# Kernel optimization log

Hardware: AMD Instinct MI355X
Metric: run time of the kernel (lower is better)

## Reference

```python
import jax, jax.numpy as jnp
import numpy as np

K = 27  # 3^3 kernel offsets for kernel_size=3, D=3
N_DOWN, N_UP = 40000, 160000
C_DOWN, C_SKIP, C_OUT = 128, 64, 96


def setup_inputs() -> dict:
    key = jax.random.key(0)
    ks = jax.random.split(key, 8)
    skip_feat = jax.random.normal(ks[0], (N_UP, C_SKIP), dtype=jnp.float32)
    down_feat = jax.random.normal(ks[1], (N_DOWN, C_DOWN), dtype=jnp.float32)
    W_deconv = jax.random.normal(ks[2], (K, C_DOWN, C_DOWN), dtype=jnp.float32) * (1.0 / np.sqrt(C_DOWN * K))
    W_conv = jax.random.normal(ks[3], (K, C_SKIP + C_DOWN, C_OUT), dtype=jnp.float32) * (1.0 / np.sqrt((C_SKIP + C_DOWN) * K))
    deconv_in_idx = jax.random.randint(ks[4], (K, N_DOWN), 0, N_DOWN, dtype=jnp.int32)
    deconv_out_idx = jax.random.randint(ks[5], (K, N_DOWN), 0, N_UP, dtype=jnp.int32)
    conv_in_idx = jax.random.randint(ks[6], (K, N_UP), 0, N_UP, dtype=jnp.int32)
    conv_out_idx = jax.random.randint(ks[7], (K, N_UP), 0, N_UP, dtype=jnp.int32)
    return {
        "skip_feat": skip_feat,
        "down_feat": down_feat,
        "W_deconv": W_deconv,
        "W_conv": W_conv,
        "deconv_in_idx": deconv_in_idx,
        "deconv_out_idx": deconv_out_idx,
        "conv_in_idx": conv_in_idx,
        "conv_out_idx": conv_out_idx,
    }


def _sparse_conv(feat, W, in_idx, out_idx, n_out):
    """ME-style sparse conv: per-offset gather -> matmul -> scatter-add."""
    out = jnp.zeros((n_out, W.shape[2]), dtype=feat.dtype)
    for k in range(W.shape[0]):  # fixed small loop over 27 kernel offsets
        msg = feat[in_idx[k]] @ W[k]          # [E_k, C_out]
        out = out.at[out_idx[k]].add(msg)
    return out


def reference(skip_feat, down_feat, W_deconv, W_conv,
              deconv_in_idx, deconv_out_idx, conv_in_idx, conv_out_idx):
    n_up = skip_feat.shape[0]
    # transposed sparse conv (stride 2) + ReLU
    up_feat = jax.nn.relu(_sparse_conv(down_feat, W_deconv, deconv_in_idx, deconv_out_idx, n_up))
    # ME.cat(up_feat, skip_feat): channel concat on shared coordinates
    cat_feat = jnp.concatenate([up_feat, skip_feat], axis=1)  # [N_up, C_down+C_skip]
    # sparse conv (stride 1) + ReLU
    net = jax.nn.relu(_sparse_conv(cat_feat, W_conv, conv_in_idx, conv_out_idx, n_up))
    return net
```

## Files before the change

### kernel.cpp

```cpp
#include <hip/hip_runtime.h>
#include <cstdint>

#define K_OFF 27
#define NDOWN 40000
#define NUP   160000
#define CDOWN 128
#define CSKIP 64
#define CCAT  192
#define COUT  96
#define TM    64
#define MT_D  5
#define MT_C  10

typedef __bf16 bf16x8 __attribute__((ext_vector_type(8)));
typedef float f32x4 __attribute__((ext_vector_type(4)));

__device__ __forceinline__ unsigned short f2b(float f) {
    unsigned int u = __float_as_uint(f);
    u += 0x7FFFu + ((u >> 16) & 1u);
    return (unsigned short)(u >> 16);
}
__device__ __forceinline__ unsigned int pk2(float a, float b) {
    return (unsigned)f2b(a) | ((unsigned)f2b(b) << 16);
}

__device__ __forceinline__ void gll16(const void* gsrc, void* ldst) {
    auto g = reinterpret_cast<const __attribute__((address_space(1))) unsigned int*>(
        reinterpret_cast<uintptr_t>(gsrc));
    auto l = reinterpret_cast<__attribute__((address_space(3))) unsigned int*>(
        reinterpret_cast<uintptr_t>(ldst));
    __builtin_amdgcn_global_load_lds(g, l, 16, 0, 0);
}


__global__ void pack_down_kernel(const float* __restrict__ down,
                                 unsigned short* __restrict__ dbf) {
    int i = blockIdx.x * 256 + threadIdx.x;
    if (i >= NDOWN * CDOWN / 8) return;
    const float4* s = (const float4*)down + (long)i * 2;
    float4 v0 = s[0], v1 = s[1];
    uint4 o;
    o.x = pk2(v0.x, v0.y); o.y = pk2(v0.z, v0.w);
    o.z = pk2(v1.x, v1.y); o.w = pk2(v1.z, v1.w);
    ((uint4*)dbf)[i] = o;
}

__global__ void pack_w_kernel(const float* __restrict__ Wd, const float* __restrict__ Wc,
                              unsigned short* __restrict__ WdT, unsigned short* __restrict__ WcT) {
    int i = blockIdx.x * 256 + threadIdx.x;
    if (i < K_OFF * CDOWN * CDOWN) {
        int k = i / (CDOWN * CDOWN), rem = i % (CDOWN * CDOWN);
        int n = rem >> 7, c = rem & 127;
        WdT[i] = f2b(Wd[((long)k * CDOWN + c) * CDOWN + n]);
    }
    if (i < K_OFF * COUT * CCAT) {
        int k = i / (COUT * CCAT), rem = i % (COUT * CCAT);
        int n = rem / CCAT, c = rem % CCAT;
        WcT[i] = f2b(Wc[((long)k * CCAT + c) * COUT + n]);
    }
}

__global__ void pack_cat_kernel(const float* __restrict__ up, const float* __restrict__ skip,
                                unsigned short* __restrict__ cat) {
    const int t = threadIdx.x;
    const int j = blockIdx.x * 8 + t / 24;
    const int s = t % 24;
    const int e0 = s * 8;
    float4 v0, v1;
    if (e0 < CDOWN) {
        const float4* src = (const float4*)(up + (long)j * CDOWN + e0);
        v0 = src[0]; v1 = src[1];
        v0.x = fmaxf(v0.x, 0.f); v0.y = fmaxf(v0.y, 0.f);
        v0.z = fmaxf(v0.z, 0.f); v0.w = fmaxf(v0.w, 0.f);
        v1.x = fmaxf(v1.x, 0.f); v1.y = fmaxf(v1.y, 0.f);
        v1.z = fmaxf(v1.z, 0.f); v1.w = fmaxf(v1.w, 0.f);
    } else {
        const float4* src = (const float4*)(skip + (long)j * CSKIP + (e0 - CDOWN));
        v0 = src[0]; v1 = src[1];
    }
    uint4 o;
    o.x = pk2(v0.x, v0.y); o.y = pk2(v0.z, v0.w);
    o.z = pk2(v1.x, v1.y); o.w = pk2(v1.z, v1.w);
    ((uint4*)(cat + (long)j * CCAT))[s] = o;
}

__global__ __launch_bounds__(256, 2)
void deconv_fast(const unsigned short* __restrict__ dbf,
                 const unsigned short* __restrict__ WdT,
                 const int* __restrict__ in_idx,
                 const int* __restrict__ out_idx,
                 float* __restrict__ up) {
    __shared__ __align__(1024) unsigned short sA[TM * CDOWN];

    const int segs = (NDOWN / TM) / MT_D;
    const int bk = blockIdx.x / segs;
    const int tile0 = (blockIdx.x % segs) * MT_D;
    const int t = threadIdx.x;
    const int wave = t >> 6, lane = t & 63;
    const int col = lane & 15, quad = lane >> 4;
    const int wm = wave & 1, wn = wave >> 1;

    int srow[4], soff[4];
#pragma unroll
    for (int i = 0; i < 4; i++) {
        int c = wave * 256 + i * 64 + lane;
        int r = c >> 4, cc = c & 15;
        srow[i] = r;
        soff[i] = (cc ^ (r & 7)) * 16;
    }

    bf16x8 b[4][4];
    {
        const unsigned short* wb = WdT + (long)bk * CDOWN * CDOWN;
#pragma unroll
        for (int kk = 0; kk < 4; kk++)
#pragma unroll
            for (int nt = 0; nt < 4; nt++)
                b[kk][nt] = *(const bf16x8*)&wb[(wn * 64 + nt * 16 + col) * CDOWN + kk * 32 + quad * 8];
    }

    const long kBase = (long)bk * NDOWN;
    const char* sAc = (const char*)sA;

    for (int tt = 0; tt < MT_D; ++tt) {
        const int rowbase = (tile0 + tt) * TM;
#pragma unroll
        for (int i = 0; i < 4; i++) {
            const int j = in_idx[kBase + rowbase + srow[i]];
            gll16((const char*)dbf + (long)j * (CDOWN * 2) + soff[i],
                  (char*)sA + (wave * 4 + i) * 1024);
        }
        __syncthreads();

        f32x4 acc[2][4];
#pragma unroll
        for (int mi = 0; mi < 2; mi++)
#pragma unroll
            for (int nt = 0; nt < 4; nt++) acc[mi][nt] = (f32x4){0.f, 0.f, 0.f, 0.f};

#pragma unroll
        for (int kk = 0; kk < 4; kk++) {
            const int ch = kk * 4 + quad;
#pragma unroll
            for (int mi = 0; mi < 2; mi++) {
                const int row = wm * 32 + mi * 16 + col;
                bf16x8 a = *(const bf16x8*)(sAc + row * 256 + ((ch ^ (row & 7)) * 16));
#pragma unroll
                for (int nt = 0; nt < 4; nt++)
                    acc[mi][nt] = __builtin_amdgcn_mfma_f32_16x16x32_bf16(a, b[kk][nt], acc[mi][nt], 0, 0, 0);
            }
        }
        __syncthreads();

#pragma unroll
        for (int mi = 0; mi < 2; mi++)
#pragma unroll
            for (int r = 0; r < 4; r++) {
                const int lrow = wm * 32 + mi * 16 + quad * 4 + r;
                const long ob = (long)out_idx[kBase + rowbase + lrow] * CDOWN;
#pragma unroll
                for (int nt = 0; nt < 4; nt++)
                    atomicAdd(&up[ob + wn * 64 + nt * 16 + col], acc[mi][nt][r]);
            }
    }
}

__global__ __launch_bounds__(256, 2)
void conv_fast(const unsigned short* __restrict__ cat,
               const unsigned short* __restrict__ WcT,
               const int* __restrict__ in_idx,
               const int* __restrict__ out_idx,
               float* __restrict__ out) {
    __shared__ __align__(1024) unsigned short sA[TM * CCAT];

    const int segs = (NUP / TM) / MT_C;
    const int bk = blockIdx.x / segs;
    const int tile0 = (blockIdx.x % segs) * MT_C;
    const int t = threadIdx.x;
    const int wave = t >> 6, lane = t & 63;
    const int col = lane & 15, quad = lane >> 4;
    const int wm = wave & 1, wn = wave >> 1;

    int srow[6], soff[6];
#pragma unroll
    for (int i = 0; i < 6; i++) {
        int c = wave * 384 + i * 64 + lane;
        int r = c / 24, cc = c % 24;
        srow[i] = r;
        soff[i] = (cc ^ (r & 7)) * 16;
    }

    bf16x8 b[6][3];
    {
        const unsigned short* wb = WcT + (long)bk * COUT * CCAT;
#pragma unroll
        for (int kk = 0; kk < 6; kk++)
#pragma unroll
            for (int nt = 0; nt < 3; nt++)
                b[kk][nt] = *(const bf16x8*)&wb[(wn * 48 + nt * 16 + col) * CCAT + kk * 32 + quad * 8];
    }

    const long kBase = (long)bk * NUP;
    const char* sAc = (const char*)sA;

    for (int tt = 0; tt < MT_C; ++tt) {
        const int rowbase = (tile0 + tt) * TM;
#pragma unroll
        for (int i = 0; i < 6; i++) {
            const int j = in_idx[kBase + rowbase + srow[i]];
            gll16((const char*)cat + (long)j * (CCAT * 2) + soff[i],
                  (char*)sA + (wave * 6 + i) * 1024);
        }
        __syncthreads();

        f32x4 acc[2][3];
#pragma unroll
        for (int mi = 0; mi < 2; mi++)
#pragma unroll
            for (int nt = 0; nt < 3; nt++) acc[mi][nt] = (f32x4){0.f, 0.f, 0.f, 0.f};

#pragma unroll
        for (int kk = 0; kk < 6; kk++) {
            const int ch = kk * 4 + quad;
#pragma unroll
            for (int mi = 0; mi < 2; mi++) {
                const int row = wm * 32 + mi * 16 + col;
                bf16x8 a = *(const bf16x8*)(sAc + row * 384 + ((ch ^ (row & 7)) * 16));
#pragma unroll
                for (int nt = 0; nt < 3; nt++)
                    acc[mi][nt] = __builtin_amdgcn_mfma_f32_16x16x32_bf16(a, b[kk][nt], acc[mi][nt], 0, 0, 0);
            }
        }
        __syncthreads();

#pragma unroll
        for (int mi = 0; mi < 2; mi++)
#pragma unroll
            for (int r = 0; r < 4; r++) {
                const int lrow = wm * 32 + mi * 16 + quad * 4 + r;
                const long ob = (long)out_idx[kBase + rowbase + lrow] * COUT;
#pragma unroll
                for (int nt = 0; nt < 3; nt++)
                    atomicAdd(&out[ob + wn * 48 + nt * 16 + col], acc[mi][nt][r]);
            }
    }
}

#define SA1 136
#define SB1 136

__global__ __launch_bounds__(256, 2)
void deconv_kernel(const float* __restrict__ down,
                   const float* __restrict__ Wd,
                   const int* __restrict__ in_idx,
                   const int* __restrict__ out_idx,
                   float* __restrict__ up) {
    __shared__ __align__(16) unsigned short sA[TM * SA1];
    __shared__ __align__(16) unsigned short sB[CDOWN * SB1];
    __shared__ int sOut[TM];

    const int tiles = NDOWN / TM;
    const int bk = blockIdx.x / tiles;
    const int tile = blockIdx.x % tiles;
    const int t = threadIdx.x;
    const long kInBase = (long)bk * NDOWN + tile * TM;

    {
        const int r = t >> 2;
        const int c0 = (t & 3) * 32;
        const int j = in_idx[kInBase + r];
        const float* src = down + (long)j * CDOWN + c0;
        unsigned short* dst = sA + r * SA1 + c0;
        #pragma unroll
        for (int c = 0; c < 32; c += 4) {
            float4 v = *(const float4*)(src + c);
            *(unsigned int*)(dst + c)     = pk2(v.x, v.y);
            *(unsigned int*)(dst + c + 2) = pk2(v.z, v.w);
        }
    }
    {
        const float* wsrc = Wd + (long)bk * CDOWN * CDOWN;
        for (int idx = t; idx < CDOWN * CDOWN; idx += 256) {
            const int kk = idx >> 7;
            const int n  = idx & 127;
            sB[n * SB1 + kk] = f2b(wsrc[idx]);
        }
    }
    if (t < TM) sOut[t] = out_idx[kInBase + t];
    __syncthreads();

    const int wave = t >> 6;
    const int lane = t & 63;
    const int col  = lane & 15;
    const int quad = lane >> 4;
    const int mrow = wave * 16 + col;

    f32x4 acc[8];
    #pragma unroll
    for (int i = 0; i < 8; i++) acc[i] = (f32x4){0.f, 0.f, 0.f, 0.f};

    #pragma unroll
    for (int k0 = 0; k0 < CDOWN; k0 += 32) {
        const int koff = k0 + quad * 8;
        bf16x8 a = *(const bf16x8*)&sA[mrow * SA1 + koff];
        #pragma unroll
        for (int nt = 0; nt < 8; nt++) {
            bf16x8 bb = *(const bf16x8*)&sB[(nt * 16 + col) * SB1 + koff];
            acc[nt] = __builtin_amdgcn_mfma_f32_16x16x32_bf16(a, bb, acc[nt], 0, 0, 0);
        }
    }
    #pragma unroll
    for (int r = 0; r < 4; r++) {
        const int lrow = wave * 16 + quad * 4 + r;
        const long obase = (long)sOut[lrow] * CDOWN;
        #pragma unroll
        for (int nt = 0; nt < 8; nt++)
            atomicAdd(&up[obase + nt * 16 + col], acc[nt][r]);
    }
}

#define SA2 200
#define SB2 200

__global__ __launch_bounds__(256, 2)
void conv_kernel(const float* __restrict__ up,
                 const float* __restrict__ skip,
                 const float* __restrict__ Wc,
                 const int* __restrict__ in_idx,
                 const int* __restrict__ out_idx,
                 float* __restrict__ out) {
    __shared__ __align__(16) unsigned short sA[TM * SA2];
    __shared__ __align__(16) unsigned short sB[COUT * SB2];
    __shared__ int sOut[TM];

    const int tiles = NUP / TM;
    const int bk = blockIdx.x / tiles;
    const int tile = blockIdx.x % tiles;
    const int t = threadIdx.x;
    const long kInBase = (long)bk * NUP + tile * TM;

    {
        const int r = t >> 2;
        const int c0 = (t & 3) * 48;
        const int j = in_idx[kInBase + r];
        const float* uprow = up + (long)j * CDOWN;
        const float* skrow = skip + (long)j * CSKIP;
        unsigned short* dst = sA + r * SA2 + c0;
        #pragma unroll
        for (int c = 0; c < 48; c += 4) {
            const int gc = c0 + c;
            float4 v;
            if (gc < CDOWN) {
                v = *(const float4*)(uprow + gc);
                v.x = fmaxf(v.x, 0.f); v.y = fmaxf(v.y, 0.f);
                v.z = fmaxf(v.z, 0.f); v.w = fmaxf(v.w, 0.f);
            } else {
                v = *(const float4*)(skrow + (gc - CDOWN));
            }
            *(unsigned int*)(dst + c)     = pk2(v.x, v.y);
            *(unsigned int*)(dst + c + 2) = pk2(v.z, v.w);
        }
    }
    {
        const float* wsrc = Wc + (long)bk * CCAT * COUT;
        for (int idx = t; idx < CCAT * COUT; idx += 256) {
            const int kk = idx / COUT;
            const int n  = idx - kk * COUT;
            sB[n * SB2 + kk] = f2b(wsrc[idx]);
        }
    }
    if (t < TM) sOut[t] = out_idx[kInBase + t];
    __syncthreads();

    const int wave = t >> 6;
    const int lane = t & 63;
    const int col  = lane & 15;
    const int quad = lane >> 4;
    const int mrow = wave * 16 + col;

    f32x4 acc[6];
    #pragma unroll
    for (int i = 0; i < 6; i++) acc[i] = (f32x4){0.f, 0.f, 0.f, 0.f};

    #pragma unroll
    for (int k0 = 0; k0 < CCAT; k0 += 32) {
        const int koff = k0 + quad * 8;
        bf16x8 a = *(const bf16x8*)&sA[mrow * SA2 + koff];
        #pragma unroll
        for (int nt = 0; nt < 6; nt++) {
            bf16x8 bb = *(const bf16x8*)&sB[(nt * 16 + col) * SB2 + koff];
            acc[nt] = __builtin_amdgcn_mfma_f32_16x16x32_bf16(a, bb, acc[nt], 0, 0, 0);
        }
    }
    #pragma unroll
    for (int r = 0; r < 4; r++) {
        const int lrow = wave * 16 + quad * 4 + r;
        const long obase = (long)sOut[lrow] * COUT;
        #pragma unroll
        for (int nt = 0; nt < 6; nt++)
            atomicAdd(&out[obase + nt * 16 + col], acc[nt][r]);
    }
}

__global__ void relu_kernel(float* __restrict__ x, int n4) {
    int i = blockIdx.x * blockDim.x + threadIdx.x;
    if (i < n4) {
        float4 v = ((float4*)x)[i];
        v.x = fmaxf(v.x, 0.f); v.y = fmaxf(v.y, 0.f);
        v.z = fmaxf(v.z, 0.f); v.w = fmaxf(v.w, 0.f);
        ((float4*)x)[i] = v;
    }
}

extern "C" void kernel_launch(void* const* d_in, const int* in_sizes, int n_in,
                              void* d_out, int out_size, void* d_ws, size_t ws_size,
                              hipStream_t stream) {
    const float* skip   = (const float*)d_in[0];
    const float* down   = (const float*)d_in[1];
    const float* Wd     = (const float*)d_in[2];
    const float* Wc     = (const float*)d_in[3];
    const int* dc_in    = (const int*)d_in[4];
    const int* dc_out   = (const int*)d_in[5];
    const int* cv_in    = (const int*)d_in[6];
    const int* cv_out   = (const int*)d_in[7];
    float* out = (float*)d_out;
    float* up  = (float*)d_ws;

    const size_t OFF_CAT = (size_t)NUP * CDOWN * 4;
    const size_t OFF_DBF = OFF_CAT + (size_t)NUP * CCAT * 2;
    const size_t OFF_WDT = OFF_DBF + (size_t)NDOWN * CDOWN * 2;
    const size_t OFF_WCT = OFF_WDT + (size_t)K_OFF * CDOWN * CDOWN * 2;
    const size_t WS_NEED = OFF_WCT + (size_t)K_OFF * COUT * CCAT * 2;

    hipMemsetAsync(up, 0, (size_t)NUP * CDOWN * sizeof(float), stream);
    hipMemsetAsync(out, 0, (size_t)out_size * sizeof(float), stream);

    if (ws_size >= WS_NEED) {
        unsigned short* catb = (unsigned short*)((char*)d_ws + OFF_CAT);
        unsigned short* dbf  = (unsigned short*)((char*)d_ws + OFF_DBF);
        unsigned short* WdT  = (unsigned short*)((char*)d_ws + OFF_WDT);
        unsigned short* WcT  = (unsigned short*)((char*)d_ws + OFF_WCT);

        pack_down_kernel<<<(NDOWN * CDOWN / 8 + 255) / 256, 256, 0, stream>>>(down, dbf);
        pack_w_kernel<<<(K_OFF * COUT * CCAT + 255) / 256, 256, 0, stream>>>(Wd, Wc, WdT, WcT);
        deconv_fast<<<K_OFF * ((NDOWN / TM) / MT_D), 256, 0, stream>>>(dbf, WdT, dc_in, dc_out, up);
        pack_cat_kernel<<<NUP / 8, 192, 0, stream>>>(up, skip, catb);
        conv_fast<<<K_OFF * ((NUP / TM) / MT_C), 256, 0, stream>>>(catb, WcT, cv_in, cv_out, out);
    } else {
        deconv_kernel<<<K_OFF * (NDOWN / TM), 256, 0, stream>>>(down, Wd, dc_in, dc_out, up);
        conv_kernel<<<K_OFF * (NUP / TM), 256, 0, stream>>>(up, skip, Wc, cv_in, cv_out, out);
    }
    relu_kernel<<<(out_size / 4 + 255) / 256, 256, 0, stream>>>(out, out_size / 4);
}
```

Measured before the change: 1.921 ms.

## Invert conv scatter into CSR gather with pre-summed inputs and fused ReLU

Builds a per-offset CSR of conv edges grouped by output row, using a histogram, a multi-level scan and a scatter. The new conv kernel walks all 27 offsets for one tile of output rows. Because the matmul is linear, it sums in fp32 all input rows that land on the same output row for an offset, then runs one MFMA pass per offset. Output is written directly with ReLU applied, so the float atomics, the output memset and the separate ReLU kernel go away. The trade-offs are extra sort kernels, reuse of the dead up buffer and the output buffer as scratch, rounding of the summed inputs to bf16, and weight reloads into LDS for every offset.

```diff
diff --git a/kernel.cpp b/kernel.cpp
--- a/kernel.cpp
+++ b/kernel.cpp
@@ -10,7 +10,7 @@
 #define COUT  96
 #define TM    64
 #define MT_D  5
-#define MT_C  10
+#define B_BINS (K_OFF * NUP)
 
 typedef __bf16 bf16x8 __attribute__((ext_vector_type(8)));
 typedef float f32x4 __attribute__((ext_vector_type(4)));
@@ -22,6 +22,9 @@
 }
 __device__ __forceinline__ unsigned int pk2(float a, float b) {
     return (unsigned)f2b(a) | ((unsigned)f2b(b) << 16);
+}
+__device__ __forceinline__ float b2f(unsigned int lo16) {
+    return __uint_as_float(lo16 << 16);
 }
 
 __device__ __forceinline__ void gll16(const void* gsrc, void* ldst) {
@@ -31,7 +34,6 @@
         reinterpret_cast<uintptr_t>(ldst));
     __builtin_amdgcn_global_load_lds(g, l, 16, 0, 0);
 }
-
 
 __global__ void pack_down_kernel(const float* __restrict__ down,
                                  unsigned short* __restrict__ dbf) {
@@ -165,85 +167,174 @@
     }
 }
 
+__global__ void hist_kernel(const int* __restrict__ cv_out, unsigned int* __restrict__ hist) {
+    const int i = blockIdx.x * 256 + threadIdx.x;
+    const int k = blockIdx.y;
+    const int j = cv_out[(long)k * NUP + i];
+    atomicAdd(&hist[(long)k * NUP + j], 1u);
+}
+
+__global__ void scan_blocks(const unsigned int* __restrict__ in, unsigned int* __restrict__ out,
+                            unsigned int* __restrict__ aux, int n) {
+    __shared__ unsigned int ls[256];
+    const int t = threadIdx.x;
+    const long base = (long)blockIdx.x * 1024 + (long)t * 4;
+    unsigned int v0 = (base     < n) ? in[base]     : 0u;
+    unsigned int v1 = (base + 1 < n) ? in[base + 1] : 0u;
+    unsigned int v2 = (base + 2 < n) ? in[base + 2] : 0u;
+    unsigned int v3 = (base + 3 < n) ? in[base + 3] : 0u;
+    const unsigned int s = v0 + v1 + v2 + v3;
+    ls[t] = s;
+    __syncthreads();
+    for (int off = 1; off < 256; off <<= 1) {
+        unsigned int x = (t >= off) ? ls[t - off] : 0u;
+        __syncthreads();
+        ls[t] += x;
+        __syncthreads();
+    }
+    const unsigned int ex = ls[t] - s;
+    if (base     < n) out[base]     = ex;
+    if (base + 1 < n) out[base + 1] = ex + v0;
+    if (base + 2 < n) out[base + 2] = ex + v0 + v1;
+    if (base + 3 < n) out[base + 3] = ex + v0 + v1 + v2;
+    if (aux != nullptr && t == 255) aux[blockIdx.x] = ls[255];
+}
+
+__global__ void addback_kernel(unsigned int* __restrict__ out, const unsigned int* __restrict__ aux, int n) {
+    const long i = (long)blockIdx.x * 256 + threadIdx.x;
+    if (i < n) out[i] += aux[i >> 10];
+}
+
+__global__ void scatter_kernel(const int* __restrict__ cv_in,
+                               const int* __restrict__ cv_out,
+                               const unsigned int* __restrict__ start,
+                               unsigned int* __restrict__ hist,
+                               unsigned int* __restrict__ entries) {
+    const int i = blockIdx.x * 256 + threadIdx.x;
+    const int k = blockIdx.y;
+    const long p = (long)k * NUP + i;
+    const int j = cv_out[p];
+    const long bin = (long)k * NUP + j;
+    const unsigned int off = atomicSub(&hist[bin], 1u) - 1u;
+    entries[start[bin] + off] = (unsigned int)cv_in[p];
+}
+
 __global__ __launch_bounds__(256, 2)
-void conv_fast(const unsigned short* __restrict__ cat,
-               const unsigned short* __restrict__ WcT,
-               const int* __restrict__ in_idx,
-               const int* __restrict__ out_idx,
-               float* __restrict__ out) {
+void conv_inv(const unsigned short* __restrict__ cat,
+              const unsigned short* __restrict__ WcT,
+              const unsigned int* __restrict__ start,
+              const unsigned int* __restrict__ entries,
+              float* __restrict__ out) {
     __shared__ __align__(1024) unsigned short sA[TM * CCAT];
-
-    const int segs = (NUP / TM) / MT_C;
-    const int bk = blockIdx.x / segs;
-    const int tile0 = (blockIdx.x % segs) * MT_C;
+    __shared__ __align__(1024) unsigned short sB[COUT * CCAT];
+
+    const int j0 = blockIdx.x * TM;
     const int t = threadIdx.x;
     const int wave = t >> 6, lane = t & 63;
     const int col = lane & 15, quad = lane >> 4;
     const int wm = wave & 1, wn = wave >> 1;
-
-    int srow[6], soff[6];
-#pragma unroll
-    for (int i = 0; i < 6; i++) {
-        int c = wave * 384 + i * 64 + lane;
-        int r = c / 24, cc = c % 24;
-        srow[i] = r;
-        soff[i] = (cc ^ (r & 7)) * 16;
-    }
-
-    bf16x8 b[6][3];
-    {
-        const unsigned short* wb = WcT + (long)bk * COUT * CCAT;
-#pragma unroll
-        for (int kk = 0; kk < 6; kk++)
+    const int r  = t >> 2;
+    const int cq = (t & 3) * 6;
+
+    f32x4 acc[2][3];
+#pragma unroll
+    for (int mi = 0; mi < 2; mi++)
+#pragma unroll
+        for (int nt = 0; nt < 3; nt++) acc[mi][nt] = (f32x4){0.f, 0.f, 0.f, 0.f};
+
+    char* sAc = (char*)sA;
+    char* sBc = (char*)sB;
+
+    for (int k = 0; k < K_OFF; k++) {
+        const long kb = (long)k * NUP;
+        const unsigned int s0 = start[kb + j0 + r];
+        const long i1 = kb + j0 + r + 1;
+        const unsigned int s1 = (i1 == (long)B_BINS) ? (unsigned int)B_BINS : start[i1];
+        const int n = (int)(s1 - s0);
+
+        uint4 ch[6];
+        if (n == 1) {
+            const unsigned int ie = entries[s0];
+            const uint4* src = (const uint4*)(cat + (long)ie * CCAT) + cq;
+#pragma unroll
+            for (int q = 0; q < 6; q++) ch[q] = src[q];
+        } else if (n == 0) {
+#pragma unroll
+            for (int q = 0; q < 6; q++) ch[q] = make_uint4(0u, 0u, 0u, 0u);
+        } else {
+            float fa[6][8];
+#pragma unroll
+            for (int q = 0; q < 6; q++)
+#pragma unroll
+                for (int e8 = 0; e8 < 8; e8++) fa[q][e8] = 0.f;
+            for (unsigned int e = s0; e < s1; e++) {
+                const unsigned int ie = entries[e];
+                const uint4* src = (const uint4*)(cat + (long)ie * CCAT) + cq;
+#pragma unroll
+                for (int q = 0; q < 6; q++) {
+                    uint4 c = src[q];
+                    fa[q][0] += b2f(c.x & 0xffffu); fa[q][1] += b2f(c.x >> 16);
+                    fa[q][2] += b2f(c.y & 0xffffu); fa[q][3] += b2f(c.y >> 16);
+                    fa[q][4] += b2f(c.z & 0xffffu); fa[q][5] += b2f(c.z >> 16);
+                    fa[q][6] += b2f(c.w & 0xffffu); fa[q][7] += b2f(c.w >> 16);
+                }
+            }
+#pragma unroll
+            for (int q = 0; q < 6; q++) {
+                ch[q].x = pk2(fa[q][0], fa[q][1]);
+                ch[q].y = pk2(fa[q][2], fa[q][3]);
+                ch[q].z = pk2(fa[q][4], fa[q][5]);
+                ch[q].w = pk2(fa[q][6], fa[q][7]);
+            }
+        }
+
+        uint4 bc[9];
+        const uint4* wsrc = (const uint4*)(WcT + (long)k * COUT * CCAT);
+#pragma unroll
+        for (int p = 0; p < 9; p++) bc[p] = wsrc[t + 256 * p];
+
+        __syncthreads();
+
+#pragma unroll
+        for (int q = 0; q < 6; q++) {
+            const int cc = cq + q;
+            *(uint4*)(sAc + r * 384 + ((cc ^ (r & 7)) << 4)) = ch[q];
+        }
+#pragma unroll
+        for (int p = 0; p < 9; p++) {
+            const int c = t + 256 * p;
+            const int nn = c / 24, cc = c % 24;
+            *(uint4*)(sBc + nn * 384 + ((cc ^ (nn & 7)) << 4)) = bc[p];
+        }
+        __syncthreads();
+
+#pragma unroll
+        for (int kk = 0; kk < 6; kk++) {
+            const int c2 = kk * 4 + quad;
+            const int row0 = wm * 32 + col;
+            const int row1 = row0 + 16;
+            bf16x8 a0 = *(const bf16x8*)(sAc + row0 * 384 + ((c2 ^ (row0 & 7)) << 4));
+            bf16x8 a1 = *(const bf16x8*)(sAc + row1 * 384 + ((c2 ^ (row1 & 7)) << 4));
+#pragma unroll
+            for (int nt = 0; nt < 3; nt++) {
+                const int bn = wn * 48 + nt * 16 + col;
+                bf16x8 bb = *(const bf16x8*)(sBc + bn * 384 + ((c2 ^ (bn & 7)) << 4));
+                acc[0][nt] = __builtin_amdgcn_mfma_f32_16x16x32_bf16(a0, bb, acc[0][nt], 0, 0, 0);
+                acc[1][nt] = __builtin_amdgcn_mfma_f32_16x16x32_bf16(a1, bb, acc[1][nt], 0, 0, 0);
+            }
+        }
+    }
+
+#pragma unroll
+    for (int mi = 0; mi < 2; mi++)
+#pragma unroll
+        for (int rr = 0; rr < 4; rr++) {
+            const int lrow = wm * 32 + mi * 16 + quad * 4 + rr;
+            float* op = out + (long)(j0 + lrow) * COUT + wn * 48 + col;
 #pragma unroll
             for (int nt = 0; nt < 3; nt++)
-                b[kk][nt] = *(const bf16x8*)&wb[(wn * 48 + nt * 16 + col) * CCAT + kk * 32 + quad * 8];
-    }
-
-    const long kBase = (long)bk * NUP;
-    const char* sAc = (const char*)sA;
-
-    for (int tt = 0; tt < MT_C; ++tt) {
-        const int rowbase = (tile0 + tt) * TM;
-#pragma unroll
-        for (int i = 0; i < 6; i++) {
-            const int j = in_idx[kBase + rowbase + srow[i]];
-            gll16((const char*)cat + (long)j * (CCAT * 2) + soff[i],
-                  (char*)sA + (wave * 6 + i) * 1024);
-        }
-        __syncthreads();
-
-        f32x4 acc[2][3];
-#pragma unroll
-        for (int mi = 0; mi < 2; mi++)
-#pragma unroll
-            for (int nt = 0; nt < 3; nt++) acc[mi][nt] = (f32x4){0.f, 0.f, 0.f, 0.f};
-
-#pragma unroll
-        for (int kk = 0; kk < 6; kk++) {
-            const int ch = kk * 4 + quad;
-#pragma unroll
-            for (int mi = 0; mi < 2; mi++) {
-                const int row = wm * 32 + mi * 16 + col;
-                bf16x8 a = *(const bf16x8*)(sAc + row * 384 + ((ch ^ (row & 7)) * 16));
-#pragma unroll
-                for (int nt = 0; nt < 3; nt++)
-                    acc[mi][nt] = __builtin_amdgcn_mfma_f32_16x16x32_bf16(a, b[kk][nt], acc[mi][nt], 0, 0, 0);
-            }
-        }
-        __syncthreads();
-
-#pragma unroll
-        for (int mi = 0; mi < 2; mi++)
-#pragma unroll
-            for (int r = 0; r < 4; r++) {
-                const int lrow = wm * 32 + mi * 16 + quad * 4 + r;
-                const long ob = (long)out_idx[kBase + rowbase + lrow] * COUT;
-#pragma unroll
-                for (int nt = 0; nt < 3; nt++)
-                    atomicAdd(&out[ob + wn * 48 + nt * 16 + col], acc[mi][nt][r]);
-            }
-    }
+                op[nt * 16] = fmaxf(acc[mi][nt][rr], 0.f);
+        }
 }
 
 #define SA1 136
@@ -433,7 +524,6 @@
     const size_t WS_NEED = OFF_WCT + (size_t)K_OFF * COUT * CCAT * 2;
 
     hipMemsetAsync(up, 0, (size_t)NUP * CDOWN * sizeof(float), stream);
-    hipMemsetAsync(out, 0, (size_t)out_size * sizeof(float), stream);
 
     if (ws_size >= WS_NEED) {
         unsigned short* catb = (unsigned short*)((char*)d_ws + OFF_CAT);
@@ -441,14 +531,31 @@
         unsigned short* WdT  = (unsigned short*)((char*)d_ws + OFF_WDT);
         unsigned short* WcT  = (unsigned short*)((char*)d_ws + OFF_WCT);
 
+        unsigned int* entriesC = (unsigned int*)d_ws;
+        unsigned int* startC   = (unsigned int*)((char*)d_ws + 17280000);
+        unsigned int* aux1     = (unsigned int*)((char*)d_ws + 34560000);
+        unsigned int* aux2     = (unsigned int*)((char*)d_ws + 34580000);
+        unsigned int* hist     = (unsigned int*)d_out;
+
         pack_down_kernel<<<(NDOWN * CDOWN / 8 + 255) / 256, 256, 0, stream>>>(down, dbf);
         pack_w_kernel<<<(K_OFF * COUT * CCAT + 255) / 256, 256, 0, stream>>>(Wd, Wc, WdT, WcT);
         deconv_fast<<<K_OFF * ((NDOWN / TM) / MT_D), 256, 0, stream>>>(dbf, WdT, dc_in, dc_out, up);
         pack_cat_kernel<<<NUP / 8, 192, 0, stream>>>(up, skip, catb);
-        conv_fast<<<K_OFF * ((NUP / TM) / MT_C), 256, 0, stream>>>(catb, WcT, cv_in, cv_out, out);
+        hipMemsetAsync(hist, 0, (size_t)B_BINS * 4, stream);
+        hist_kernel<<<dim3(NUP / 256, K_OFF), 256, 0, stream>>>(cv_out, hist);
+        const int nblk1 = (B_BINS + 1023) / 1024;
+        const int nblk2 = (nblk1 + 1023) / 1024;
+        scan_blocks<<<nblk1, 256, 0, stream>>>(hist, startC, aux1, B_BINS);
+        scan_blocks<<<nblk2, 256, 0, stream>>>(aux1, aux1, aux2, nblk1);
+        scan_blocks<<<1, 256, 0, stream>>>(aux2, aux2, nullptr, nblk2);
+        addback_kernel<<<(nblk1 + 255) / 256, 256, 0, stream>>>(aux1, aux2, nblk1);
+        addback_kernel<<<(B_BINS + 255) / 256, 256, 0, stream>>>(startC, aux1, B_BINS);
+        scatter_kernel<<<dim3(NUP / 256, K_OFF), 256, 0, stream>>>(cv_in, cv_out, startC, hist, entriesC);
+        conv_inv<<<NUP / TM, 256, 0, stream>>>(catb, WcT, startC, entriesC, out);
     } else {
+        hipMemsetAsync(out, 0, (size_t)out_size * sizeof(float), stream);
         deconv_kernel<<<K_OFF * (NDOWN / TM), 256, 0, stream>>>(down, Wd, dc_in, dc_out, up);
         conv_kernel<<<K_OFF * (NUP / TM), 256, 0, stream>>>(up, skip, Wc, cv_in, cv_out, out);
-    }
-    relu_kernel<<<(out_size / 4 + 255) / 256, 256, 0, stream>>>(out, out_size / 4);
-}
+        relu_kernel<<<(out_size / 4 + 255) / 256, 256, 0, stream>>>(out, out_size / 4);
+    }
+}
```

Result: slower. 2.197 ms (+14.4%).
